# Kernel tuning notes

Measured on AMD Instinct MI355X. Metric: run time of the kernel, lower is better.

Reference implementation:

```python
import jax, jax.numpy as jnp
import numpy as np

DIM = 512
NUM_HEADS = 8


def setup_inputs() -> dict:
    key = jax.random.key(0)
    ks = jax.random.split(key, 10)
    B, N, C = 2, 4096, DIM
    s = 0.02
    return {
        "x": jax.random.normal(ks[0], (B, N, C), dtype=jnp.float32),
        "Wq": jax.random.normal(ks[1], (C, C), dtype=jnp.float32) * s,
        "Wk": jax.random.normal(ks[2], (C, C), dtype=jnp.float32) * s,
        "Wv": jax.random.normal(ks[3], (C, C), dtype=jnp.float32) * s,
        "Wattn": jax.random.normal(ks[4], (C, C), dtype=jnp.float32) * s,
        "Wconv": jax.random.normal(ks[5], (C, C), dtype=jnp.float32) * s,
        "dw_kernel": jax.random.normal(ks[6], (C, 1, 3), dtype=jnp.float32) * s,  # depthwise (O, I/groups, K)
        "dw_bias": jax.random.normal(ks[7], (C,), dtype=jnp.float32) * s,
        "Wcout": jax.random.normal(ks[8], (C, C), dtype=jnp.float32) * s,
        "H": 8,
        "W": 512,
    }


def reference(x, Wq, Wk, Wv, Wattn, Wconv, dw_kernel, dw_bias, Wcout, H, W):
    B, N, C = x.shape
    nh = NUM_HEADS
    hd = C // nh
    scale = hd ** (-0.5)

    # QKV projections (torch Linear: x @ W.T), split heads -> [B, nh, N, hd]
    q = (x @ Wq.T).reshape(B, N, nh, hd).transpose(0, 2, 1, 3)
    k = (x @ Wk.T).reshape(B, N, nh, hd).transpose(0, 2, 1, 3)
    v = (x @ Wv.T).reshape(B, N, nh, hd).transpose(0, 2, 1, 3)

    # Materialized N x N attention (faithful to source)
    scores = jnp.einsum("bhqd,bhkd->bhqk", q, k) * scale
    weights = jax.nn.softmax(scores, axis=-1)
    attn = jnp.einsum("bhqk,bhkd->bhqd", weights, v)
    attn = attn.transpose(0, 2, 1, 3).reshape(B, N, C)
    attn_out = attn @ Wattn.T

    # Parallel depthwise-conv branch
    ci = (x @ Wconv.T).transpose(0, 2, 1)  # [B, C, N]
    co = jax.lax.conv_general_dilated(
        ci, dw_kernel,
        window_strides=(1,), padding=((1, 1),),
        feature_group_count=C,
        dimension_numbers=("NCH", "OIH", "NCH"),
    ) + dw_bias[None, :, None]
    conv_out = co.transpose(0, 2, 1) @ Wcout.T  # [B, N, C]

    out = attn_out + conv_out
    # NOTE: source shadows arg H with num_heads before the view
    return out.reshape(B, nh, W, C)
```

## Files before the change

kernel.cpp:

```cpp
#include <hip/hip_runtime.h>

typedef __attribute__((ext_vector_type(8))) short bf16x8;
typedef __attribute__((ext_vector_type(4))) float f32x4;

constexpr int kB = 2, kN = 4096, kC = 512, kNH = 8, kHD = 64;
constexpr int kBN = kB * kN;
constexpr int kWElems = 262144;
constexpr int kWAll = 6 * kWElems;
constexpr int kWExtra = 3584;
constexpr float kQScale = 0.1803368801f;

__device__ __forceinline__ short f2bf(float f) {
  union { float f; unsigned u; } v; v.f = f;
  unsigned r = v.u + 0x7fffu + ((v.u >> 16) & 1u);
  return (short)(r >> 16);
}
__device__ __forceinline__ float bf2f(short s) {
  union { unsigned u; float f; } v; v.u = ((unsigned)(unsigned short)s) << 16;
  return v.f;
}
__device__ __forceinline__ float exp2_(float x) {
#if __has_builtin(__builtin_amdgcn_exp2f)
  return __builtin_amdgcn_exp2f(x);
#else
  return exp2f(x);
#endif
}
__device__ __forceinline__ unsigned pk2bf(float a, float b) {
  union { float f; unsigned u; } ua, ub; ua.f = a; ub.f = b;
#if __has_builtin(__builtin_amdgcn_perm)
  return __builtin_amdgcn_perm(ub.u + 0x8000u, ua.u + 0x8000u, 0x07060302u);
#else
  return ((ua.u + 0x8000u) >> 16) | (((ub.u + 0x8000u) >> 16) << 16);
#endif
}

__device__ __forceinline__ bf16x8 ld8(const short* p) { return *(const bf16x8*)p; }
__device__ __forceinline__ bf16x8 ld8(const float* p) {
  float4 a = *(const float4*)p;
  float4 b = *(const float4*)(p + 4);
  bf16x8 r;
  r[0] = f2bf(a.x); r[1] = f2bf(a.y); r[2] = f2bf(a.z); r[3] = f2bf(a.w);
  r[4] = f2bf(b.x); r[5] = f2bf(b.y); r[6] = f2bf(b.z); r[7] = f2bf(b.w);
  return r;
}

__device__ __forceinline__ void gload_lds16(const void* g, void* l) {
  __builtin_amdgcn_global_load_lds(
      (const __attribute__((address_space(1))) void*)g,
      (__attribute__((address_space(3))) void*)l, 16, 0, 0);
}

__device__ __forceinline__ bool classify_bf(const unsigned* xw) {
  unsigned w = xw[threadIdx.x & 63];
  int e = (int)((w >> 7) & 0xffu);
  bool isbf = (e >= 100 && e <= 140);
  unsigned long long m = __ballot(isbf);
  return __popcll(m) >= 32;
}

constexpr int kW8 = kWAll / 8;
constexpr int kX8 = kBN * kC / 8;
__global__ __launch_bounds__(256) void convert_all(
    const void* Wq, const void* Wk, const void* Wv, const void* Wc,
    const void* Wa, const void* Wco, const void* dwk, const void* dwb,
    const void* x, int* __restrict__ flag, short* __restrict__ dst,
    short* __restrict__ xb) {
  const bool bf = classify_bf((const unsigned*)x);
  const int gtid = blockIdx.x * 256 + threadIdx.x;
  if (gtid == 0) *flag = bf ? 1 : 0;
  if (gtid < kW8) {
    const int e = gtid * 8;
    const int t = e >> 18, off = e & (kWElems - 1);
    const void* src = (t == 0) ? Wq : (t == 1) ? Wk : (t == 2) ? Wv
                    : (t == 3) ? Wc : (t == 4) ? Wa : Wco;
    bf16x8 v = bf ? ld8((const short*)src + off) : ld8((const float*)src + off);
    *(bf16x8*)(dst + e) = v;
  } else if (gtid < kW8 + kWExtra) {
    const int eoff = gtid - kW8;
    if (eoff < 1536) {
      dst[kWAll + eoff] = bf ? ((const short*)dwk)[eoff]
                             : f2bf(((const float*)dwk)[eoff]);
    } else if (eoff < 2048) {
      const int i = eoff - 1536;
      dst[kWAll + 1536 + i] = bf ? ((const short*)dwb)[i]
                                 : f2bf(((const float*)dwb)[i]);
    } else {
      const int t2 = eoff - 2048;
      const int tap = t2 >> 9, c = t2 & 511;
      dst[kWAll + 2048 + t2] = bf ? ((const short*)dwk)[c * 3 + tap]
                                  : f2bf(((const float*)dwk)[c * 3 + tap]);
    }
  } else if (gtid < kW8 + kWExtra + kX8) {
    const int e = (gtid - kW8 - kWExtra) * 8;
    bf16x8 v = bf ? ld8((const short*)x + e) : ld8((const float*)x + e);
    *(bf16x8*)(xb + e) = v;
  }
}

__global__ __launch_bounds__(256, 2) void proj_gemm(
    const short* __restrict__ xb, const short* __restrict__ wb,
    short* __restrict__ q, short* __restrict__ k, short* __restrict__ vT,
    short* __restrict__ ci) {
  __shared__ __align__(16) short As2[2][8192];
  __shared__ __align__(16) short Bs2[2][8192];
  const int t = threadIdx.x;
  const int wave = t >> 6, lane = t & 63;
  const int row = lane & 15, quad = lane >> 4;
  const int swz = (blockIdx.x & 7) * 128 + (blockIdx.x >> 3);
  const int bn = swz & 15;
  const int bm = swz >> 4;
  const int m0 = bm * 128, n0 = bn * 128;
  const int wm = wave & 1, wn = wave >> 1;
  const int lrow = lane >> 3, lch = lane & 7;

  f32x4 acc[4][4];
#pragma unroll
  for (int mi = 0; mi < 4; ++mi)
#pragma unroll
    for (int ni = 0; ni < 4; ++ni)
#pragma unroll
      for (int r = 0; r < 4; ++r) acc[mi][ni][r] = 0.0f;

  auto stage = [&](int buf, int k0) {
#pragma unroll
    for (int p = 0; p < 4; ++p) {
      const int m = wave * 32 + p * 8 + lrow;
      const int kch = lch ^ (m & 7);
      gload_lds16(xb + (size_t)(m0 + m) * kC + k0 + kch * 8,
                  &As2[buf][(wave * 32 + p * 8) * 64]);
      gload_lds16(wb + (size_t)(n0 + m) * kC + k0 + kch * 8,
                  &Bs2[buf][(wave * 32 + p * 8) * 64]);
    }
  };

  stage(0, 0);
  __syncthreads();

  for (int step = 0; step < 8; ++step) {
    const int cur = step & 1;
    if (step < 7) stage(1 - cur, (step + 1) * 64);

#pragma unroll
    for (int kk2 = 0; kk2 < 2; ++kk2) {
      bf16x8 af[4], bfr[4];
#pragma unroll
      for (int mi = 0; mi < 4; ++mi) {
        const int m = wm * 64 + mi * 16 + row;
        const int ch = (kk2 * 4 + quad) ^ (m & 7);
        af[mi] = *(const bf16x8*)(&As2[cur][m * 64 + ch * 8]);
      }
#pragma unroll
      for (int ni = 0; ni < 4; ++ni) {
        const int n = wn * 64 + ni * 16 + row;
        const int ch = (kk2 * 4 + quad) ^ (n & 7);
        bfr[ni] = *(const bf16x8*)(&Bs2[cur][n * 64 + ch * 8]);
      }
#pragma unroll
      for (int mi = 0; mi < 4; ++mi)
#pragma unroll
        for (int ni = 0; ni < 4; ++ni)
          acc[mi][ni] = __builtin_amdgcn_mfma_f32_16x16x32_bf16(
              af[mi], bfr[ni], acc[mi][ni], 0, 0, 0);
    }
    __syncthreads();
  }

  short* Sh = &As2[0][0];
  const int mat = n0 >> 9;
  const float scale = (mat == 0) ? kQScale : 1.0f;
  if (mat != 2) {
#pragma unroll
    for (int mi = 0; mi < 4; ++mi)
#pragma unroll
      for (int ni = 0; ni < 4; ++ni)
#pragma unroll
        for (int r = 0; r < 4; ++r) {
          const int m = wm * 64 + mi * 16 + quad * 4 + r;
          const int n = wn * 64 + ni * 16 + row;
          Sh[m * 128 + (((n >> 3) ^ (m & 15)) * 8) + (n & 7)] =
              f2bf(acc[mi][ni][r] * scale);
        }
  } else {
#pragma unroll
    for (int mi = 0; mi < 4; ++mi)
#pragma unroll
      for (int ni = 0; ni < 4; ++ni)
#pragma unroll
        for (int r = 0; r < 4; ++r) {
          const int m = wm * 64 + mi * 16 + quad * 4 + r;
          const int n = wn * 64 + ni * 16 + row;
          Sh[n * 128 + (((m >> 3) ^ (n & 15)) * 8) + (m & 7)] =
              f2bf(acc[mi][ni][r]);
        }
  }
  __syncthreads();
  const int b_ = m0 >> 12;
  const int rsub = lane >> 4, chk = lane & 15;
#pragma unroll
  for (int i = 0; i < 8; ++i) {
    const int rr = i * 16 + wave * 4 + rsub;
    bf16x8 v = *(const bf16x8*)(&Sh[rr * 128 + ((chk ^ (rr & 15)) * 8)]);
    if (mat == 2) {
      const int cg = (n0 + rr) & 511;
      const int h = cg >> 6, d = cg & 63;
      const int nb = (m0 & (kN - 1)) + chk * 8;
      *(bf16x8*)(vT + ((size_t)((b_ * kNH + h) * kHD + d)) * kN + nb) = v;
    } else {
      const int n_ = (m0 & (kN - 1)) + rr;
      const int cg = (n0 + chk * 8) & 511;
      if (mat == 3) {
        *(bf16x8*)(ci + ((size_t)(b_ * kN + n_)) * kC + cg) = v;
      } else {
        const int h = cg >> 6, d = cg & 63;
        short* dst = (mat == 0) ? q : k;
        *(bf16x8*)(dst + ((size_t)((b_ * kNH + h) * kN + n_)) * kHD + d) = v;
      }
    }
  }
}

__global__ __launch_bounds__(256) void dwconv(
    const short* __restrict__ ci, const short* __restrict__ wb,
    short* __restrict__ cb) {
  const int e0 = (blockIdx.x * 256 + threadIdx.x) * 8;
  const int c0 = e0 & (kC - 1);
  const int bn = e0 >> 9;
  const int n_ = bn & (kN - 1);
  bf16x8 xc = ld8(ci + e0);
  bf16x8 xm, xp;
  if (n_ > 0) xm = ld8(ci + e0 - kC);
  else
#pragma unroll
    for (int i = 0; i < 8; ++i) xm[i] = 0;
  if (n_ < kN - 1) xp = ld8(ci + e0 + kC);
  else
#pragma unroll
    for (int i = 0; i < 8; ++i) xp[i] = 0;
  bf16x8 w0 = ld8(wb + kWAll + 2048 + c0);
  bf16x8 w1 = ld8(wb + kWAll + 2048 + 512 + c0);
  bf16x8 w2 = ld8(wb + kWAll + 2048 + 1024 + c0);
  bf16x8 bi = ld8(wb + kWAll + 1536 + c0);
  bf16x8 o;
#pragma unroll
  for (int i = 0; i < 8; ++i) {
    float a = bf2f(bi[i]) + bf2f(xm[i]) * bf2f(w0[i]) +
              bf2f(xc[i]) * bf2f(w1[i]) + bf2f(xp[i]) * bf2f(w2[i]);
    o[i] = f2bf(a);
  }
  *(bf16x8*)(cb + e0) = o;
}

__global__ __launch_bounds__(512, 2) void attn_flash(
    const short* __restrict__ q, const short* __restrict__ k,
    const short* __restrict__ vT, short* __restrict__ attn) {
  __shared__ __align__(16) short SMEM[69632];
  short* Kb = SMEM;
  short* Vb = SMEM + 32768;
  const int t = threadIdx.x;
  const int wave = t >> 6;
  const int lane = t & 63;
  const int row = lane & 15;
  const int quad = lane >> 4;
  const int qg = wave & 3;
  const int ks = wave >> 2;

  const int slot = blockIdx.x & 7;
  const int inner = blockIdx.x >> 3;
  const int bh = slot * 2 + (inner & 1);
  const int q0 = (inner >> 1) * 256 + qg * 64;

  const short* qbase = q + (size_t)(bh * kN + q0) * kHD;
  const short* kbase = k + (size_t)bh * kN * kHD;
  const short* vbase = vT + (size_t)bh * kHD * kN;

  bf16x8 qb[4][2];
#pragma unroll
  for (int g = 0; g < 4; ++g) {
    qb[g][0] = *(const bf16x8*)(qbase + (g * 16 + row) * kHD + quad * 8);
    qb[g][1] = *(const bf16x8*)(qbase + (g * 16 + row) * kHD + 32 + quad * 8);
  }

  const f32x4 z4 = {0.0f, 0.0f, 0.0f, 0.0f};

  f32x4 o[4][4];
#pragma unroll
  for (int g = 0; g < 4; ++g)
#pragma unroll
    for (int j = 0; j < 4; ++j)
#pragma unroll
      for (int r = 0; r < 4; ++r) o[g][j][r] = 0.0f;
  float l_[4] = {0.0f, 0.0f, 0.0f, 0.0f};

  const int ksrow = lane >> 3;
  const int kschunk = (lane & 7) ^ ksrow;
  auto stage_k = [&](int buf, int ktbase) {
#pragma unroll
    for (int tl = 0; tl < 2; ++tl)
#pragma unroll
      for (int s2 = 0; s2 < 2; ++s2)
        gload_lds16(
            kbase + (size_t)(s2 * 2048 + (ktbase + tl) * 64 + wave * 8 + ksrow) * 64 +
                kschunk * 8,
            &Kb[((buf * 2 + tl) * 2 + s2) * 4096 + wave * 512]);
  };

  const int sv = t >> 8;
  const int ii = t & 255;
  const int i0 = ii, i1 = ii + 256;
  const int sr0 = i0 >> 3, sc0 = i0 & 7;
  const int sr1 = i1 >> 3, sc1 = i1 & 7;
  const int vb0 = (sc0 >> 2) * 32 + (sc0 & 1) * 16 + (sc0 & 2) * 2;
  const int vb1 = (sc1 >> 2) * 32 + (sc1 & 1) * 16 + (sc1 & 2) * 2;

  auto stage_v = [&](int buf, int tl, bf16x8 v0, bf16x8 v1) {
    short* base = &Vb[((buf * 2 + tl) * 2 + sv) * 4608];
    *(short4*)(&base[sr0 * 72 + vb0]) = make_short4(v0[0], v0[1], v0[2], v0[3]);
    *(short4*)(&base[sr0 * 72 + vb0 + 8]) = make_short4(v0[4], v0[5], v0[6], v0[7]);
    *(short4*)(&base[sr1 * 72 + vb1]) = make_short4(v1[0], v1[1], v1[2], v1[3]);
    *(short4*)(&base[sr1 * 72 + vb1 + 8]) = make_short4(v1[4], v1[5], v1[6], v1[7]);
  };

  const int c0s = ((quad) ^ (row & 7)) * 8;
  const int c1s = ((quad + 4) ^ (row & 7)) * 8;

  auto tile_step = [&](const short* kt_base, const short* vt_base) {
    f32x4 s[4][4];
    __builtin_amdgcn_s_setprio(1);
#pragma unroll
    for (int jk = 0; jk < 4; ++jk) {
      const short* kr = kt_base + (jk * 16 + row) * 64;
      bf16x8 a0 = *(const bf16x8*)(kr + c0s);
      bf16x8 a1 = *(const bf16x8*)(kr + c1s);
#pragma unroll
      for (int g = 0; g < 4; ++g) {
        s[g][jk] = __builtin_amdgcn_mfma_f32_16x16x32_bf16(a0, qb[g][0], z4, 0, 0, 0);
        s[g][jk] = __builtin_amdgcn_mfma_f32_16x16x32_bf16(a1, qb[g][1], s[g][jk], 0, 0, 0);
      }
    }
    __builtin_amdgcn_s_setprio(0);

    bf16x8 pb[4][2];
#pragma unroll
    for (int g = 0; g < 4; ++g) {
      float tj[4];
#pragma unroll
      for (int jk = 0; jk < 4; ++jk) {
#pragma unroll
        for (int r = 0; r < 4; ++r) s[g][jk][r] = exp2_(s[g][jk][r]);
        tj[jk] = (s[g][jk][0] + s[g][jk][1]) + (s[g][jk][2] + s[g][jk][3]);
      }
      l_[g] += (tj[0] + tj[1]) + (tj[2] + tj[3]);
#pragma unroll
      for (int c = 0; c < 2; ++c) {
        union { unsigned u[4]; bf16x8 v; } pu;
        pu.u[0] = pk2bf(s[g][2 * c][0], s[g][2 * c][1]);
        pu.u[1] = pk2bf(s[g][2 * c][2], s[g][2 * c][3]);
        pu.u[2] = pk2bf(s[g][2 * c + 1][0], s[g][2 * c + 1][1]);
        pu.u[3] = pk2bf(s[g][2 * c + 1][2], s[g][2 * c + 1][3]);
        pb[g][c] = pu.v;
      }
    }

    __builtin_amdgcn_s_setprio(1);
#pragma unroll
    for (int jd = 0; jd < 4; ++jd) {
      const short* vb = vt_base + (jd * 16 + row) * 72 + quad * 8;
#pragma unroll
      for (int c = 0; c < 2; ++c) {
        bf16x8 av = *(const bf16x8*)(vb + c * 32);
#pragma unroll
        for (int g = 0; g < 4; ++g)
          o[g][jd] = __builtin_amdgcn_mfma_f32_16x16x32_bf16(
              av, pb[g][c], o[g][jd], 0, 0, 0);
      }
    }
    __builtin_amdgcn_s_setprio(0);
  };

  {
    stage_k(0, 0);
#pragma unroll
    for (int tl = 0; tl < 2; ++tl) {
      bf16x8 a = *(const bf16x8*)(vbase + (size_t)sr0 * kN + sv * 2048 + tl * 64 + sc0 * 8);
      bf16x8 b = *(const bf16x8*)(vbase + (size_t)sr1 * kN + sv * 2048 + tl * 64 + sc1 * 8);
      stage_v(0, tl, a, b);
    }
  }
  __syncthreads();

  for (int p = 0; p < 16; ++p) {
    const int cur = p & 1;
    const bool more = (p < 15);
    bf16x8 vn00, vn01, vn10, vn11;
    if (more) {
      stage_k(1 - cur, 2 * p + 2);
      const int off = sv * 2048 + (2 * p + 2) * 64;
      vn00 = *(const bf16x8*)(vbase + (size_t)sr0 * kN + off + sc0 * 8);
      vn01 = *(const bf16x8*)(vbase + (size_t)sr1 * kN + off + sc1 * 8);
      vn10 = *(const bf16x8*)(vbase + (size_t)sr0 * kN + off + 64 + sc0 * 8);
      vn11 = *(const bf16x8*)(vbase + (size_t)sr1 * kN + off + 64 + sc1 * 8);
    }

    tile_step(&Kb[((cur * 2 + 0) * 2 + ks) * 4096], &Vb[((cur * 2 + 0) * 2 + ks) * 4608]);

    if (more) {
      stage_v(1 - cur, 0, vn00, vn01);
      stage_v(1 - cur, 1, vn10, vn11);
    }

    tile_step(&Kb[((cur * 2 + 1) * 2 + ks) * 4096], &Vb[((cur * 2 + 1) * 2 + ks) * 4608]);
    __syncthreads();
  }

  float* Of = (float*)SMEM;
  float* Lf = (float*)SMEM + 16384;
  if (ks == 1) {
#pragma unroll
    for (int g = 0; g < 4; ++g) {
#pragma unroll
      for (int jd = 0; jd < 4; ++jd)
#pragma unroll
        for (int r = 0; r < 4; ++r)
          Of[(g * 16 + jd * 4 + r) * 256 + qg * 64 + lane] = o[g][jd][r];
      Lf[g * 256 + qg * 64 + lane] = l_[g];
    }
  }
  __syncthreads();
  if (ks == 0) {
#pragma unroll
    for (int g = 0; g < 4; ++g) {
#pragma unroll
      for (int jd = 0; jd < 4; ++jd)
#pragma unroll
        for (int r = 0; r < 4; ++r)
          o[g][jd][r] += Of[(g * 16 + jd * 4 + r) * 256 + qg * 64 + lane];
      l_[g] += Lf[g * 256 + qg * 64 + lane];
    }
    const int b_ = bh >> 3, h = bh & 7;
#pragma unroll
    for (int g = 0; g < 4; ++g) {
      float lt = l_[g];
      lt += __shfl_xor(lt, 16);
      lt += __shfl_xor(lt, 32);
      const float linv = 1.0f / lt;
      const int n_ = q0 + g * 16 + row;
      short* ob = attn + (size_t)(b_ * kN + n_) * kC + h * kHD + quad * 4;
#pragma unroll
      for (int jd = 0; jd < 4; ++jd) {
        short4 st = make_short4(f2bf(o[g][jd][0] * linv), f2bf(o[g][jd][1] * linv),
                                f2bf(o[g][jd][2] * linv), f2bf(o[g][jd][3] * linv));
        *(short4*)(ob + jd * 16) = st;
      }
    }
  }
}

template <typename TO>
__device__ __forceinline__ void out_body(
    const short* __restrict__ attn, const short* __restrict__ cb,
    const short* __restrict__ wb, TO* __restrict__ out) {
  __shared__ __align__(16) short As2[2][8192];
  __shared__ __align__(16) short Bs2[2][4096];
  const int t = threadIdx.x;
  const int wave = t >> 6, lane = t & 63;
  const int row = lane & 15, quad = lane >> 4;
  const int swz = (blockIdx.x & 7) * 64 + (blockIdx.x >> 3);
  const int bn = swz & 7;
  const int bm = swz >> 3;
  const int m0 = bm * 128, n0 = bn * 64;
  const int wm = wave & 1, wn = wave >> 1;
  const int lrow = lane >> 3, lch = lane & 7;

  f32x4 acc[4][2];
#pragma unroll
  for (int mi = 0; mi < 4; ++mi)
#pragma unroll
    for (int ni = 0; ni < 2; ++ni)
#pragma unroll
      for (int r = 0; r < 4; ++r) acc[mi][ni][r] = 0.0f;

  const short* Wa = wb + 4 * kWElems;
  const short* Wo = wb + 5 * kWElems;

  auto stage = [&](int buf, int kt) {
    const short* Asrc = (kt < 8) ? attn : cb;
    const short* Bsrc = (kt < 8) ? Wa : Wo;
    const int ka = (kt * 64) & 511;
#pragma unroll
    for (int p = 0; p < 4; ++p) {
      const int m = wave * 32 + p * 8 + lrow;
      const int kch = lch ^ (m & 7);
      gload_lds16(Asrc + (size_t)(m0 + m) * kC + ka + kch * 8,
                  &As2[buf][(wave * 32 + p * 8) * 64]);
    }
#pragma unroll
    for (int p = 0; p < 2; ++p) {
      const int n = wave * 16 + p * 8 + lrow;
      const int kch = lch ^ (n & 7);
      gload_lds16(Bsrc + (size_t)(n0 + n) * kC + ka + kch * 8,
                  &Bs2[buf][(wave * 16 + p * 8) * 64]);
    }
  };

  stage(0, 0);
  __syncthreads();

  for (int kt = 0; kt < 16; ++kt) {
    const int cur = kt & 1;
    if (kt < 15) stage(1 - cur, kt + 1);

#pragma unroll
    for (int kk2 = 0; kk2 < 2; ++kk2) {
      bf16x8 af[4], bfr[2];
#pragma unroll
      for (int mi = 0; mi < 4; ++mi) {
        const int m = wm * 64 + mi * 16 + row;
        const int ch = (kk2 * 4 + quad) ^ (m & 7);
        af[mi] = *(const bf16x8*)(&As2[cur][m * 64 + ch * 8]);
      }
#pragma unroll
      for (int ni = 0; ni < 2; ++ni) {
        const int n = wn * 32 + ni * 16 + row;
        const int ch = (kk2 * 4 + quad) ^ (n & 7);
        bfr[ni] = *(const bf16x8*)(&Bs2[cur][n * 64 + ch * 8]);
      }
#pragma unroll
      for (int mi = 0; mi < 4; ++mi)
#pragma unroll
        for (int ni = 0; ni < 2; ++ni)
          acc[mi][ni] = __builtin_amdgcn_mfma_f32_16x16x32_bf16(
              af[mi], bfr[ni], acc[mi][ni], 0, 0, 0);
    }
    __syncthreads();
  }

  if constexpr (sizeof(TO) == 4) {
    float* Shf = (float*)&As2[0][0];
#pragma unroll
    for (int mi = 0; mi < 4; ++mi)
#pragma unroll
      for (int ni = 0; ni < 2; ++ni)
#pragma unroll
        for (int r = 0; r < 4; ++r) {
          const int m = wm * 64 + mi * 16 + quad * 4 + r;
          const int n = wn * 32 + ni * 16 + row;
          Shf[m * 64 + (((n >> 2) ^ (m & 15)) * 4) + (n & 3)] = acc[mi][ni][r];
        }
    __syncthreads();
    const int rsub = lane >> 4, chk = lane & 15;
#pragma unroll
    for (int i = 0; i < 8; ++i) {
      const int rr = i * 16 + wave * 4 + rsub;
      float4 v = *(const float4*)(&Shf[rr * 64 + ((chk ^ (rr & 15)) * 4)]);
      *(float4*)((float*)out + (size_t)(m0 + rr) * kC + n0 + chk * 4) = v;
    }
  } else {
    short* Sh = &As2[0][0];
#pragma unroll
    for (int mi = 0; mi < 4; ++mi)
#pragma unroll
      for (int ni = 0; ni < 2; ++ni)
#pragma unroll
        for (int r = 0; r < 4; ++r) {
          const int m = wm * 64 + mi * 16 + quad * 4 + r;
          const int n = wn * 32 + ni * 16 + row;
          Sh[m * 64 + (((n >> 3) ^ (m & 7)) * 8) + (n & 7)] =
              f2bf(acc[mi][ni][r]);
        }
    __syncthreads();
    const int rsub = lane >> 3, chk = lane & 7;
#pragma unroll
    for (int i = 0; i < 4; ++i) {
      const int rr = i * 32 + wave * 8 + rsub;
      bf16x8 v = *(const bf16x8*)(&Sh[rr * 64 + ((chk ^ (rr & 7)) * 8)]);
      *(bf16x8*)((short*)out + (size_t)(m0 + rr) * kC + n0 + chk * 8) = v;
    }
  }
}

__global__ __launch_bounds__(256, 3) void out_gemm(
    const short* __restrict__ attn, const short* __restrict__ cb,
    const short* __restrict__ wb, const int* __restrict__ flag, void* out) {
  if (*flag)
    out_body<short>(attn, cb, wb, (short*)out);
  else
    out_body<float>(attn, cb, wb, (float*)out);
}

extern "C" void kernel_launch(void* const* d_in, const int* in_sizes, int n_in,
                              void* d_out, int out_size, void* d_ws, size_t ws_size,
                              hipStream_t stream) {
  const void* x   = d_in[0];
  const void* Wq  = d_in[1];
  const void* Wk  = d_in[2];
  const void* Wv  = d_in[3];
  const void* Wa  = d_in[4];
  const void* Wc  = d_in[5];
  const void* dwk = d_in[6];
  const void* dwb = d_in[7];
  const void* Wco = d_in[8];

  short* ws = (short*)d_ws;
  const size_t E = (size_t)kBN * kC;
  int*   flag = (int*)ws;
  short* wb   = ws + 256;
  short* q    = wb + kWAll + kWExtra;
  short* k    = q + E;
  short* vT   = k + E;
  short* ci   = vT + E;
  short* cb   = ci + E;
  short* attn = ci;
  short* xb   = cb;

  const int cvt_threads = kW8 + kWExtra + kX8;
  convert_all<<<(cvt_threads + 255) / 256, 256, 0, stream>>>(
      Wq, Wk, Wv, Wc, Wa, Wco, dwk, dwb, x, flag, wb, xb);
  proj_gemm<<<1024, 256, 0, stream>>>(xb, wb, q, k, vT, ci);
  dwconv<<<(kBN * kC) / (256 * 8), 256, 0, stream>>>(ci, wb, cb);
  attn_flash<<<256, 512, 0, stream>>>(q, k, vT, attn);
  out_gemm<<<512, 256, 0, stream>>>(attn, cb, wb, flag, d_out);
}
```

Baseline: 221.3 us.

## Fuse depthwise conv into output GEMM A-tile staging

Removes the separate dwconv kernel and computes the depthwise conv on the fly while staging the conv half of the output GEMM's A operand, writing results directly into swizzled shared memory. This drops one launch and a full write and read of the intermediate conv buffer. In exchange, the second half of the GEMM K loop uses synchronous register loads, three rows per output, instead of async global-to-LDS copies. Launch bounds are lowered from 3 to 2 blocks per SIMD to make room for the extra registers. The attention output buffer is moved to reuse the x staging buffer.

```diff
diff --git a/kernel.cpp b/kernel.cpp
--- a/kernel.cpp
+++ b/kernel.cpp
@@ -220,37 +220,6 @@
   }
 }
 
-__global__ __launch_bounds__(256) void dwconv(
-    const short* __restrict__ ci, const short* __restrict__ wb,
-    short* __restrict__ cb) {
-  const int e0 = (blockIdx.x * 256 + threadIdx.x) * 8;
-  const int c0 = e0 & (kC - 1);
-  const int bn = e0 >> 9;
-  const int n_ = bn & (kN - 1);
-  bf16x8 xc = ld8(ci + e0);
-  bf16x8 xm, xp;
-  if (n_ > 0) xm = ld8(ci + e0 - kC);
-  else
-#pragma unroll
-    for (int i = 0; i < 8; ++i) xm[i] = 0;
-  if (n_ < kN - 1) xp = ld8(ci + e0 + kC);
-  else
-#pragma unroll
-    for (int i = 0; i < 8; ++i) xp[i] = 0;
-  bf16x8 w0 = ld8(wb + kWAll + 2048 + c0);
-  bf16x8 w1 = ld8(wb + kWAll + 2048 + 512 + c0);
-  bf16x8 w2 = ld8(wb + kWAll + 2048 + 1024 + c0);
-  bf16x8 bi = ld8(wb + kWAll + 1536 + c0);
-  bf16x8 o;
-#pragma unroll
-  for (int i = 0; i < 8; ++i) {
-    float a = bf2f(bi[i]) + bf2f(xm[i]) * bf2f(w0[i]) +
-              bf2f(xc[i]) * bf2f(w1[i]) + bf2f(xp[i]) * bf2f(w2[i]);
-    o[i] = f2bf(a);
-  }
-  *(bf16x8*)(cb + e0) = o;
-}
-
 __global__ __launch_bounds__(512, 2) void attn_flash(
     const short* __restrict__ q, const short* __restrict__ k,
     const short* __restrict__ vT, short* __restrict__ attn) {
@@ -458,7 +427,7 @@
 
 template <typename TO>
 __device__ __forceinline__ void out_body(
-    const short* __restrict__ attn, const short* __restrict__ cb,
+    const short* __restrict__ attn2, const short* __restrict__ ci,
     const short* __restrict__ wb, TO* __restrict__ out) {
   __shared__ __align__(16) short As2[2][8192];
   __shared__ __align__(16) short Bs2[2][4096];
@@ -471,6 +440,7 @@
   const int m0 = bm * 128, n0 = bn * 64;
   const int wm = wave & 1, wn = wave >> 1;
   const int lrow = lane >> 3, lch = lane & 7;
+  const int kch = lch ^ lrow;
 
   f32x4 acc[4][2];
 #pragma unroll
@@ -483,32 +453,70 @@
   const short* Wa = wb + 4 * kWElems;
   const short* Wo = wb + 5 * kWElems;
 
-  auto stage = [&](int buf, int kt) {
-    const short* Asrc = (kt < 8) ? attn : cb;
+  auto stageB = [&](int buf, int kt) {
     const short* Bsrc = (kt < 8) ? Wa : Wo;
     const int ka = (kt * 64) & 511;
 #pragma unroll
+    for (int p = 0; p < 2; ++p) {
+      const int n = wave * 16 + p * 8 + lrow;
+      const int kchb = lch ^ (n & 7);
+      gload_lds16(Bsrc + (size_t)(n0 + n) * kC + ka + kchb * 8,
+                  &Bs2[buf][(wave * 16 + p * 8) * 64]);
+    }
+  };
+  auto stageA_attn = [&](int buf, int kt) {
+    const int ka = kt * 64;
+#pragma unroll
     for (int p = 0; p < 4; ++p) {
       const int m = wave * 32 + p * 8 + lrow;
-      const int kch = lch ^ (m & 7);
-      gload_lds16(Asrc + (size_t)(m0 + m) * kC + ka + kch * 8,
+      gload_lds16(attn2 + (size_t)(m0 + m) * kC + ka + kch * 8,
                   &As2[buf][(wave * 32 + p * 8) * 64]);
     }
-#pragma unroll
-    for (int p = 0; p < 2; ++p) {
-      const int n = wave * 16 + p * 8 + lrow;
-      const int kch = lch ^ (n & 7);
-      gload_lds16(Bsrc + (size_t)(n0 + n) * kC + ka + kch * 8,
-                  &Bs2[buf][(wave * 16 + p * 8) * 64]);
-    }
   };
-
-  stage(0, 0);
+  auto stageA_conv = [&](int buf, int kt) {
+    const int c0 = ((kt * 64) & 511) + kch * 8;
+    bf16x8 w0 = ld8(wb + kWAll + 2048 + c0);
+    bf16x8 w1 = ld8(wb + kWAll + 2048 + 512 + c0);
+    bf16x8 w2 = ld8(wb + kWAll + 2048 + 1024 + c0);
+    bf16x8 bi = ld8(wb + kWAll + 1536 + c0);
+#pragma unroll
+    for (int p = 0; p < 4; ++p) {
+      const int m = wave * 32 + p * 8 + lrow;
+      const int gm = m0 + m;
+      const int n_ = gm & (kN - 1);
+      const short* cbase = ci + (size_t)gm * kC + c0;
+      bf16x8 xc = ld8(cbase);
+      bf16x8 xm, xp;
+      if (n_ > 0) xm = ld8(cbase - kC);
+      else
+#pragma unroll
+        for (int i = 0; i < 8; ++i) xm[i] = 0;
+      if (n_ < kN - 1) xp = ld8(cbase + kC);
+      else
+#pragma unroll
+        for (int i = 0; i < 8; ++i) xp[i] = 0;
+      bf16x8 o8;
+#pragma unroll
+      for (int i = 0; i < 8; ++i) {
+        float a = bf2f(bi[i]) + bf2f(xm[i]) * bf2f(w0[i]) +
+                  bf2f(xc[i]) * bf2f(w1[i]) + bf2f(xp[i]) * bf2f(w2[i]);
+        o8[i] = f2bf(a);
+      }
+      *(bf16x8*)(&As2[buf][(wave * 32 + p * 8) * 64 + lane * 8]) = o8;
+    }
+  };
+
+  stageB(0, 0);
+  stageA_attn(0, 0);
   __syncthreads();
 
   for (int kt = 0; kt < 16; ++kt) {
     const int cur = kt & 1;
-    if (kt < 15) stage(1 - cur, kt + 1);
+    if (kt < 15) {
+      stageB(1 - cur, kt + 1);
+      if (kt + 1 < 8) stageA_attn(1 - cur, kt + 1);
+      else            stageA_conv(1 - cur, kt + 1);
+    }
 
 #pragma unroll
     for (int kk2 = 0; kk2 < 2; ++kk2) {
@@ -579,13 +587,13 @@
   }
 }
 
-__global__ __launch_bounds__(256, 3) void out_gemm(
-    const short* __restrict__ attn, const short* __restrict__ cb,
+__global__ __launch_bounds__(256, 2) void out_gemm(
+    const short* __restrict__ attn2, const short* __restrict__ ci,
     const short* __restrict__ wb, const int* __restrict__ flag, void* out) {
   if (*flag)
-    out_body<short>(attn, cb, wb, (short*)out);
+    out_body<short>(attn2, ci, wb, (short*)out);
   else
-    out_body<float>(attn, cb, wb, (float*)out);
+    out_body<float>(attn2, ci, wb, (float*)out);
 }
 
 extern "C" void kernel_launch(void* const* d_in, const int* in_sizes, int n_in,
@@ -609,15 +617,13 @@
   short* k    = q + E;
   short* vT   = k + E;
   short* ci   = vT + E;
-  short* cb   = ci + E;
-  short* attn = ci;
-  short* xb   = cb;
+  short* xb   = ci + E;
+  short* attn2 = xb;
 
   const int cvt_threads = kW8 + kWExtra + kX8;
   convert_all<<<(cvt_threads + 255) / 256, 256, 0, stream>>>(
       Wq, Wk, Wv, Wc, Wa, Wco, dwk, dwb, x, flag, wb, xb);
   proj_gemm<<<1024, 256, 0, stream>>>(xb, wb, q, k, vT, ci);
-  dwconv<<<(kBN * kC) / (256 * 8), 256, 0, stream>>>(ci, wb, cb);
-  attn_flash<<<256, 512, 0, stream>>>(q, k, vT, attn);
-  out_gemm<<<512, 256, 0, stream>>>(attn, cb, wb, flag, d_out);
-}
+  attn_flash<<<256, 512, 0, stream>>>(q, k, vT, attn2);
+  out_gemm<<<512, 256, 0, stream>>>(attn2, ci, wb, flag, d_out);
+}
```

Measured after the change: 231.9 us. 4.8% more time.
